# Kernel optimization log

Measured on AMD Instinct MI355X. Metric: run time of the kernel, lower is better.

The kernel has to match this reference:

```python
import jax, jax.numpy as jnp
import numpy as np

# Adaptive-LIF constants (Yin et al. spiking RNN, which this thesis repo builds on)
B_J0 = 0.01    # baseline threshold
BETA = 1.8     # adaptation strength
GAMMA = 0.5    # surrogate gradient scale
LENS = 0.5     # surrogate gaussian width
HIGHT = 0.15   # multi-gaussian side-lobe height
SCALE = 6.0    # side-lobe width multiplier


def _gaussian(x, mu, sigma):
    return jnp.exp(-((x - mu) ** 2) / (2.0 * sigma ** 2)) / (jnp.sqrt(2.0 * jnp.pi) * sigma)


@jax.custom_vjp
def spike_fn(v):
    # Heaviside spike with multi-gaussian surrogate gradient
    return (v > 0).astype(v.dtype)

def _spike_fwd(v):
    return spike_fn(v), v

def _spike_bwd(v, g):
    sg = (_gaussian(v, 0.0, LENS) * (1.0 + HIGHT)
          - _gaussian(v, LENS, SCALE * LENS) * HIGHT
          - _gaussian(v, -LENS, SCALE * LENS) * HIGHT)
    return (g * sg * GAMMA,)

spike_fn.defvjp(_spike_fwd, _spike_bwd)


def setup_inputs() -> dict:
    key = jax.random.key(0)
    ks = jax.random.split(key, 16)
    B, S, C, H, O = 256, 250, 700, 256, 20

    def lin(k, fan_in, shape):  # nn.Linear default init
        lim = 1.0 / np.sqrt(fan_in)
        return jax.random.uniform(k, shape, jnp.float32, -lim, lim)

    def tau(k, mean, std, shape):
        return jnp.clip(mean + std * jax.random.normal(k, shape, jnp.float32), 1.0, None)

    return {
        "x": jax.random.normal(ks[0], (B, S, C), jnp.float32),
        # forward spiking cell (tauM ~ N(20, ~5), tauAdp ~ N(200, ~50))
        "W_in_f": lin(ks[1], C, (C, H)), "b_in_f": lin(ks[2], C, (H,)),
        "W_rec_f": lin(ks[3], H, (H, H)), "b_rec_f": lin(ks[4], H, (H,)),
        "tau_m_f": tau(ks[5], 20.0, 5.0, (H,)),
        "tau_adp_f": tau(ks[6], 200.0, 50.0, (H,)),
        # backward spiking cell
        "W_in_b": lin(ks[7], C, (C, H)), "b_in_b": lin(ks[8], C, (H,)),
        "W_rec_b": lin(ks[9], H, (H, H)), "b_rec_b": lin(ks[10], H, (H,)),
        "tau_m_b": tau(ks[11], 20.0, 5.0, (H,)),
        "tau_adp_b": tau(ks[12], 200.0, 50.0, (H,)),
        # readout leaky integrator over concat(fw, bw) = 512 -> 20, tauM ~ N(3, 1)
        "W_out": lin(ks[13], 2 * H, (2 * H, O)), "b_out": lin(ks[14], 2 * H, (O,)),
        "tau_m_out": tau(ks[15], 3.0, 1.0, (O,)),
    }


def reference(x, W_in_f, b_in_f, W_rec_f, b_rec_f, tau_m_f, tau_adp_f,
              W_in_b, b_in_b, W_rec_b, b_rec_b, tau_m_b, tau_adp_b,
              W_out, b_out, tau_m_out):
    B, S, C = x.shape
    H = W_in_f.shape[1]
    O = W_out.shape[1]

    alpha_f = jnp.exp(-1.0 / tau_m_f); ro_f = jnp.exp(-1.0 / tau_adp_f)
    alpha_b = jnp.exp(-1.0 / tau_m_b); ro_b = jnp.exp(-1.0 / tau_adp_b)
    alpha_o = jnp.exp(-1.0 / tau_m_out)

    # Batch the feed-forward input projections over all timesteps: [S, B, H]
    proj_f = jnp.einsum("bsc,ch->sbh", x, W_in_f) + b_in_f
    proj_b = jnp.einsum("bsc,ch->sbh", x[:, ::-1], W_in_b) + b_in_b

    def cell(in_t, mem, spk, bb, W_rec, b_rec, alpha, ro):
        # mem_update_adp: adaptive threshold LIF
        d = in_t + spk @ W_rec + b_rec
        bb = ro * bb + (1.0 - ro) * spk
        thr = B_J0 + BETA * bb
        mem = mem * alpha + (1.0 - alpha) * d - thr * spk
        spk = spike_fn(mem - thr)
        return mem, spk, bb

    def step(carry, xs):
        mem_f, spk_f, bb_f, mem_b, spk_b, bb_b, mem_o = carry
        in_f, in_b = xs
        mem_f, spk_f, bb_f = cell(in_f, mem_f, spk_f, bb_f, W_rec_f, b_rec_f, alpha_f, ro_f)
        mem_b, spk_b, bb_b = cell(in_b, mem_b, spk_b, bb_b, W_rec_b, b_rec_b, alpha_b, ro_b)
        # readout integrator over concat(fw, bw) spikes (method=1 integrates every step)
        merged = jnp.concatenate([spk_f, spk_b], axis=-1)
        mem_o = mem_o * alpha_o + (1.0 - alpha_o) * (merged @ W_out + b_out)
        return (mem_f, spk_f, bb_f, mem_b, spk_b, bb_b, mem_o), None

    z = jnp.zeros((B, H), x.dtype)
    b0 = jnp.full((B, H), B_J0, x.dtype)
    carry0 = (z, z, b0, z, z, b0, jnp.zeros((B, O), x.dtype))
    carry, _ = jax.lax.scan(step, carry0, (proj_f, proj_b))
    return jax.nn.log_softmax(carry[-1], axis=-1)
```

## Files before the change

kernel.cpp:

```cpp
#include <hip/hip_runtime.h>
#include <cstdint>
#include <cstddef>

#define S_LEN 250
#define BATCH 256
#define CIN   700
#define HID   256
#define OUT_N 20
#define KSTEPS 22

typedef __attribute__((ext_vector_type(8))) short bf16x8;
typedef __attribute__((ext_vector_type(4))) float f32x4;

__device__ __forceinline__ ushort f2bf_rne(float f) {
    uint u = __float_as_uint(f);
    uint r = (u + 0x7FFFu + ((u >> 16) & 1u)) >> 16;
    return (ushort)r;
}
__device__ __forceinline__ float bf2f(ushort h) {
    return __uint_as_float(((uint)h) << 16);
}

__global__ __launch_bounds__(256) void proj_mfma(
    const float* __restrict__ x,
    const float* __restrict__ Wf, const float* __restrict__ Wb,
    const float* __restrict__ biasf, const float* __restrict__ biasb,
    float* __restrict__ P)
{
    __shared__ ushort AsH[128][40];
    __shared__ ushort AsL[128][40];
    __shared__ ushort BsH[128][40];
    __shared__ ushort BsL[128][40];

    const int nt = blockIdx.x;
    const int mt = blockIdx.y;
    const int m0 = mt * 128;
    const float* W   = (nt < 2) ? Wf : Wb;
    const float* bia = (nt < 2) ? biasf : biasb;
    const int wc0 = (nt & 1) * 128;

    const int tid  = threadIdx.x;
    const int lane = tid & 63;
    const int wv   = tid >> 6;
    const int wr   = wv >> 1;
    const int wc   = wv & 1;
    const int l15  = lane & 15;
    const int l4   = lane >> 4;

    const int as  = tid & 7;
    const int arr = tid >> 3;
    const int bcol = tid & 127;
    const int bkh  = tid >> 7;

    f32x4 acc[4][4];
#pragma unroll
    for (int i = 0; i < 4; i++)
#pragma unroll
        for (int j = 0; j < 4; j++)
            acc[i][j] = (f32x4){0.f, 0.f, 0.f, 0.f};

    for (int kt = 0; kt < KSTEPS; kt++) {
        const int k0 = kt * 32;

        float4 av[4];
        const int ka = k0 + as * 4;
        const bool aok = (ka + 3) < CIN;
#pragma unroll
        for (int i = 0; i < 4; i++) {
            av[i] = make_float4(0.f, 0.f, 0.f, 0.f);
            if (aok)
                av[i] = *(const float4*)&x[(size_t)(m0 + arr + 32 * i) * CIN + ka];
        }
        float bv[16];
#pragma unroll
        for (int j = 0; j < 16; j++) {
            const int kb = k0 + bkh * 16 + j;
            bv[j] = (kb < CIN) ? W[(size_t)kb * HID + wc0 + bcol] : 0.f;
        }

        __syncthreads();

#pragma unroll
        for (int i = 0; i < 4; i++) {
            const int row = arr + 32 * i;
            ushort4 h, l;
            h.x = f2bf_rne(av[i].x); l.x = f2bf_rne(__fsub_rn(av[i].x, bf2f(h.x)));
            h.y = f2bf_rne(av[i].y); l.y = f2bf_rne(__fsub_rn(av[i].y, bf2f(h.y)));
            h.z = f2bf_rne(av[i].z); l.z = f2bf_rne(__fsub_rn(av[i].z, bf2f(h.z)));
            h.w = f2bf_rne(av[i].w); l.w = f2bf_rne(__fsub_rn(av[i].w, bf2f(h.w)));
            *(ushort4*)&AsH[row][as * 4] = h;
            *(ushort4*)&AsL[row][as * 4] = l;
        }
#pragma unroll
        for (int q = 0; q < 4; q++) {
            ushort4 h, l;
            float v0 = bv[q * 4 + 0], v1 = bv[q * 4 + 1];
            float v2 = bv[q * 4 + 2], v3 = bv[q * 4 + 3];
            h.x = f2bf_rne(v0); l.x = f2bf_rne(__fsub_rn(v0, bf2f(h.x)));
            h.y = f2bf_rne(v1); l.y = f2bf_rne(__fsub_rn(v1, bf2f(h.y)));
            h.z = f2bf_rne(v2); l.z = f2bf_rne(__fsub_rn(v2, bf2f(h.z)));
            h.w = f2bf_rne(v3); l.w = f2bf_rne(__fsub_rn(v3, bf2f(h.w)));
            *(ushort4*)&BsH[bcol][bkh * 16 + q * 4] = h;
            *(ushort4*)&BsL[bcol][bkh * 16 + q * 4] = l;
        }
        __syncthreads();

        bf16x8 aH[4], aL[4], bH[4], bL[4];
#pragma unroll
        for (int f = 0; f < 4; f++) {
            aH[f] = *(const bf16x8*)&AsH[wr * 64 + f * 16 + l15][l4 * 8];
            aL[f] = *(const bf16x8*)&AsL[wr * 64 + f * 16 + l15][l4 * 8];
            bH[f] = *(const bf16x8*)&BsH[wc * 64 + f * 16 + l15][l4 * 8];
            bL[f] = *(const bf16x8*)&BsL[wc * 64 + f * 16 + l15][l4 * 8];
        }
#pragma unroll
        for (int fr = 0; fr < 4; fr++)
#pragma unroll
            for (int fc = 0; fc < 4; fc++) {
                acc[fr][fc] = __builtin_amdgcn_mfma_f32_16x16x32_bf16(
                    aH[fr], bH[fc], acc[fr][fc], 0, 0, 0);
                acc[fr][fc] = __builtin_amdgcn_mfma_f32_16x16x32_bf16(
                    aH[fr], bL[fc], acc[fr][fc], 0, 0, 0);
                acc[fr][fc] = __builtin_amdgcn_mfma_f32_16x16x32_bf16(
                    aL[fr], bH[fc], acc[fr][fc], 0, 0, 0);
            }
    }

#pragma unroll
    for (int fc = 0; fc < 4; fc++) {
        const float bvs = bia[wc0 + wc * 64 + fc * 16 + l15];
#pragma unroll
        for (int fr = 0; fr < 4; fr++) {
#pragma unroll
            for (int j = 0; j < 4; j++) {
                const int row = m0 + wr * 64 + fr * 16 + l4 * 4 + j;
                P[(size_t)row * 512 + nt * 128 + wc * 64 + fc * 16 + l15] =
                    __fadd_rn(acc[fr][fc][j], bvs);
            }
        }
    }
}

__global__ __launch_bounds__(512, 2) void scan_mfma(
    const float* __restrict__ P,
    const float* __restrict__ Wrecf, const float* __restrict__ brecf,
    const float* __restrict__ taumf, const float* __restrict__ tauaf,
    const float* __restrict__ Wrecb, const float* __restrict__ brecb,
    const float* __restrict__ taumb, const float* __restrict__ tauab,
    const float* __restrict__ Wout, const float* __restrict__ taumo,
    float* __restrict__ Pst)
{
    const int g  = blockIdx.x;
    const int d  = blockIdx.y;
    const int b0 = g * 16;
    const bool fw = (d == 0);

    const int tid  = threadIdx.x;
    const int lane = tid & 63;
    const int w    = tid >> 6;
    const int l15  = lane & 15;
    const int l4   = lane >> 4;

    __shared__ ushort Sp[2][16][264];

    {
        ushort* p = &Sp[0][0][0];
        for (int i = tid; i < 2 * 16 * 264; i += 512) p[i] = 0;
    }

    const float* Wrec = fw ? Wrecf : Wrecb;

    bf16x8 whf[8][2], wlf[8][2];
#pragma unroll
    for (int kt = 0; kt < 8; kt++)
#pragma unroll
        for (int ct = 0; ct < 2; ct++) {
            const int c = w * 32 + ct * 16 + l15;
#pragma unroll
            for (int j = 0; j < 8; j++) {
                const float v = Wrec[(size_t)(kt * 32 + l4 * 8 + j) * HID + c];
                const ushort h = f2bf_rne(v);
                const ushort l = f2bf_rne(__fsub_rn(v, bf2f(h)));
                whf[kt][ct][j] = (short)h;
                wlf[kt][ct][j] = (short)l;
            }
        }

    bf16x8 woh[2], wol[2];
#pragma unroll
    for (int t = 0; t < 2; t++) {
        const int o = t * 16 + l15;
#pragma unroll
        for (int j = 0; j < 8; j++) {
            float v = 0.f;
            if (o < OUT_N)
                v = Wout[(size_t)(d * HID + w * 32 + l4 * 8 + j) * OUT_N + o];
            const ushort h = f2bf_rne(v);
            const ushort l = f2bf_rne(__fsub_rn(v, bf2f(h)));
            woh[t][j] = (short)h;
            wol[t][j] = (short)l;
        }
    }

    float alpha_[2], ro_[2], omA_[2], omR_[2], brc_[2];
#pragma unroll
    for (int t = 0; t < 2; t++) {
        const int c = w * 32 + t * 16 + l15;
        alpha_[t] = expf(__fdiv_rn(-1.f, fw ? taumf[c] : taumb[c]));
        ro_[t]    = expf(__fdiv_rn(-1.f, fw ? tauaf[c] : tauab[c]));
        omA_[t]   = __fsub_rn(1.f, alpha_[t]);
        omR_[t]   = __fsub_rn(1.f, ro_[t]);
        brc_[t]   = fw ? brecf[c] : brecb[c];
    }
    float ao_[2], omo_[2];
#pragma unroll
    for (int t = 0; t < 2; t++) {
        const int o = t * 16 + l15;
        if (o < OUT_N) {
            ao_[t]  = expf(__fdiv_rn(-1.f, taumo[o]));
            omo_[t] = __fsub_rn(1.f, ao_[t]);
        } else { ao_[t] = 0.f; omo_[t] = 0.f; }
    }

    float mem[2][4], bbv[2][4], spkv[2][4], z[2][4];
#pragma unroll
    for (int t = 0; t < 2; t++)
#pragma unroll
        for (int j = 0; j < 4; j++) {
            mem[t][j] = 0.f; bbv[t][j] = 0.01f; spkv[t][j] = 0.f; z[t][j] = 0.f;
        }

    float pv[2][4];
    {
        const int srow = fw ? 0 : (S_LEN - 1);
#pragma unroll
        for (int t = 0; t < 2; t++)
#pragma unroll
            for (int j = 0; j < 4; j++)
                pv[t][j] = P[((size_t)(b0 + l4 * 4 + j) * S_LEN + srow) * 512
                             + d * HID + w * 32 + t * 16 + l15];
    }

    for (int s = 0; s < S_LEN; s++) {
        const int cur = s & 1, prev = cur ^ 1;

        float pvn[2][4];
        {
            const int sn  = s + 1;
            const int srn = fw ? (sn < S_LEN ? sn : S_LEN - 1)
                               : (sn < S_LEN ? (S_LEN - 1 - sn) : 0);
#pragma unroll
            for (int t = 0; t < 2; t++)
#pragma unroll
                for (int j = 0; j < 4; j++)
                    pvn[t][j] = P[((size_t)(b0 + l4 * 4 + j) * S_LEN + srn) * 512
                                  + d * HID + w * 32 + t * 16 + l15];
        }

        __syncthreads();

        f32x4 acc[2];
        acc[0] = (f32x4){0.f, 0.f, 0.f, 0.f};
        acc[1] = (f32x4){0.f, 0.f, 0.f, 0.f};
#pragma unroll
        for (int kt = 0; kt < 8; kt++) {
            const bf16x8 a = *(const bf16x8*)&Sp[prev][l15][kt * 32 + l4 * 8];
            acc[0] = __builtin_amdgcn_mfma_f32_16x16x32_bf16(a, whf[kt][0], acc[0], 0, 0, 0);
            acc[0] = __builtin_amdgcn_mfma_f32_16x16x32_bf16(a, wlf[kt][0], acc[0], 0, 0, 0);
            acc[1] = __builtin_amdgcn_mfma_f32_16x16x32_bf16(a, whf[kt][1], acc[1], 0, 0, 0);
            acc[1] = __builtin_amdgcn_mfma_f32_16x16x32_bf16(a, wlf[kt][1], acc[1], 0, 0, 0);
        }

#pragma unroll
        for (int t = 0; t < 2; t++) {
#pragma unroll
            for (int j = 0; j < 4; j++) {
                const float dd = __fadd_rn(__fadd_rn(pv[t][j], acc[t][j]), brc_[t]);
                bbv[t][j] = __fadd_rn(__fmul_rn(ro_[t], bbv[t][j]),
                                      __fmul_rn(omR_[t], spkv[t][j]));
                const float thr = __fadd_rn(0.01f, __fmul_rn(1.8f, bbv[t][j]));
                mem[t][j] = __fsub_rn(
                    __fadd_rn(__fmul_rn(mem[t][j], alpha_[t]),
                              __fmul_rn(omA_[t], dd)),
                    __fmul_rn(thr, spkv[t][j]));
                const bool sp = __fsub_rn(mem[t][j], thr) > 0.f;
                spkv[t][j] = sp ? 1.f : 0.f;
                Sp[cur][l4 * 4 + j][w * 32 + t * 16 + l15] =
                    sp ? (ushort)0x3F80 : (ushort)0;
            }
        }

        asm volatile("s_waitcnt lgkmcnt(0)" ::: "memory");
        __builtin_amdgcn_sched_barrier(0);

        {
            const bf16x8 ar = *(const bf16x8*)&Sp[cur][l15][w * 32 + l4 * 8];
            f32x4 S0 = (f32x4){0.f, 0.f, 0.f, 0.f};
            f32x4 S1 = (f32x4){0.f, 0.f, 0.f, 0.f};
            S0 = __builtin_amdgcn_mfma_f32_16x16x32_bf16(ar, woh[0], S0, 0, 0, 0);
            S0 = __builtin_amdgcn_mfma_f32_16x16x32_bf16(ar, wol[0], S0, 0, 0, 0);
            S1 = __builtin_amdgcn_mfma_f32_16x16x32_bf16(ar, woh[1], S1, 0, 0, 0);
            S1 = __builtin_amdgcn_mfma_f32_16x16x32_bf16(ar, wol[1], S1, 0, 0, 0);
#pragma unroll
            for (int j = 0; j < 4; j++) {
                z[0][j] = __fmaf_rn(ao_[0], z[0][j], __fmul_rn(omo_[0], S0[j]));
                z[1][j] = __fmaf_rn(ao_[1], z[1][j], __fmul_rn(omo_[1], S1[j]));
            }
        }

#pragma unroll
        for (int t = 0; t < 2; t++)
#pragma unroll
            for (int j = 0; j < 4; j++) pv[t][j] = pvn[t][j];
    }

    __syncthreads();

    float* stash = Pst + ((size_t)b0 * S_LEN) * 512 + d * HID;
#pragma unroll
    for (int j = 0; j < 4; j++) {
        const int r = l4 * 4 + j;
        const int idx0 = w * 320 + r * 16 + l15;
        stash[(size_t)(idx0 >> 8) * 512 + (idx0 & 255)] = z[0][j];
        if (l15 < 4) {
            const int idx1 = w * 320 + 256 + r * 4 + l15;
            stash[(size_t)(idx1 >> 8) * 512 + (idx1 & 255)] = z[1][j];
        }
    }
}

__global__ __launch_bounds__(64) void merge_out(
    const float* __restrict__ Pst, const float* __restrict__ bout,
    const float* __restrict__ taumo, float* __restrict__ out)
{
    const int bb = blockIdx.x;
    const int o  = threadIdx.x;
    const int g  = bb >> 4, r = bb & 15;

    float val = 0.f, v = -3.0e38f;
    if (o < OUT_N) {
        float tot = 0.f;
#pragma unroll
        for (int d2 = 0; d2 < 2; d2++) {
            const float* stash = Pst + ((size_t)(g * 16) * S_LEN) * 512 + d2 * HID;
#pragma unroll
            for (int w2 = 0; w2 < 8; w2++) {
                const int idx = (o < 16) ? (w2 * 320 + r * 16 + o)
                                         : (w2 * 320 + 256 + r * 4 + (o - 16));
                tot = __fadd_rn(tot, stash[(size_t)(idx >> 8) * 512 + (idx & 255)]);
            }
        }
        const float aS = expf(__fdiv_rn(-(float)S_LEN, taumo[o]));
        val = __fadd_rn(tot, __fmul_rn(bout[o], __fsub_rn(1.f, aS)));
        v = val;
    }
    float mx = v;
#pragma unroll
    for (int d2 = 1; d2 < 64; d2 <<= 1)
        mx = fmaxf(mx, __shfl_xor(mx, d2, 64));
    float e = (o < OUT_N) ? expf(__fsub_rn(val, mx)) : 0.f;
#pragma unroll
    for (int d2 = 1; d2 < 64; d2 <<= 1)
        e += __shfl_xor(e, d2, 64);
    if (o < OUT_N)
        out[(size_t)bb * OUT_N + o] =
            __fsub_rn(__fsub_rn(val, mx), logf(e));
}

extern "C" void kernel_launch(void* const* d_in, const int* in_sizes, int n_in,
                              void* d_out, int out_size, void* d_ws, size_t ws_size,
                              hipStream_t stream) {
    const float* x         = (const float*)d_in[0];
    const float* W_in_f    = (const float*)d_in[1];
    const float* b_in_f    = (const float*)d_in[2];
    const float* W_rec_f   = (const float*)d_in[3];
    const float* b_rec_f   = (const float*)d_in[4];
    const float* tau_m_f   = (const float*)d_in[5];
    const float* tau_adp_f = (const float*)d_in[6];
    const float* W_in_b    = (const float*)d_in[7];
    const float* b_in_b    = (const float*)d_in[8];
    const float* W_rec_b   = (const float*)d_in[9];
    const float* b_rec_b   = (const float*)d_in[10];
    const float* tau_m_b   = (const float*)d_in[11];
    const float* tau_adp_b = (const float*)d_in[12];
    const float* W_out     = (const float*)d_in[13];
    const float* b_out     = (const float*)d_in[14];
    const float* tau_m_o   = (const float*)d_in[15];
    float* out = (float*)d_out;
    float* P   = (float*)d_ws;

    proj_mfma<<<dim3(4, 500), dim3(256), 0, stream>>>(
        x, W_in_f, W_in_b, b_in_f, b_in_b, P);
    scan_mfma<<<dim3(16, 2), dim3(512), 0, stream>>>(
        P, W_rec_f, b_rec_f, tau_m_f, tau_adp_f,
        W_rec_b, b_rec_b, tau_m_b, tau_adp_b,
        W_out, tau_m_o, P);
    merge_out<<<dim3(BATCH), dim3(64), 0, stream>>>(
        P, b_out, tau_m_o, out);
}
```

Measured before the change: 517.7 us.

## Defer readout MFMA by one step, split accumulators, swizzle LDS, prefetch two steps

Moves the readout MFMA for step s-1 into step s's recurrent MFMA block, reading the previous spike buffer. This removes the separate lgkmcnt wait and sched barrier from the serial critical path, with one extra readout applied after the loop. It also splits the hi/lo accumulators to shorten MFMA dependency chains and swaps the padded LDS layout for an XOR swizzle to avoid bank conflicts. The P projection prefetch now runs two steps ahead to hide global load latency. The cost is more registers and some restructuring risk around the z update order, where the readout now lags by one step.

```diff
diff --git a/kernel.cpp b/kernel.cpp
--- a/kernel.cpp
+++ b/kernel.cpp
@@ -161,11 +161,11 @@
     const int l15  = lane & 15;
     const int l4   = lane >> 4;
 
-    __shared__ ushort Sp[2][16][264];
+    __shared__ ushort Sp[2][16][256];
 
     {
         ushort* p = &Sp[0][0][0];
-        for (int i = tid; i < 2 * 16 * 264; i += 512) p[i] = 0;
+        for (int i = tid; i < 2 * 16 * 256; i += 512) p[i] = 0;
     }
 
     const float* Wrec = fw ? Wrecf : Wrecb;
@@ -230,52 +230,96 @@
             mem[t][j] = 0.f; bbv[t][j] = 0.01f; spkv[t][j] = 0.f; z[t][j] = 0.f;
         }
 
-    float pv[2][4];
-    {
-        const int srow = fw ? 0 : (S_LEN - 1);
-#pragma unroll
-        for (int t = 0; t < 2; t++)
-#pragma unroll
-            for (int j = 0; j < 4; j++)
-                pv[t][j] = P[((size_t)(b0 + l4 * 4 + j) * S_LEN + srow) * 512
-                             + d * HID + w * 32 + t * 16 + l15];
-    }
+#define PROW(S_) (fw ? (((S_) < S_LEN) ? (S_) : (S_LEN - 1)) \
+                     : (((S_) < S_LEN) ? (S_LEN - 1 - (S_)) : 0))
+#define PLOAD(dst, S_) do {                                            \
+        const int srow_ = PROW(S_);                                    \
+        _Pragma("unroll")                                              \
+        for (int t_ = 0; t_ < 2; t_++)                                 \
+            _Pragma("unroll")                                          \
+            for (int j_ = 0; j_ < 4; j_++)                             \
+                dst[t_][j_] = P[((size_t)(b0 + l4 * 4 + j_) * S_LEN + srow_) * 512 \
+                                + d * HID + w * 32 + t_ * 16 + l15];   \
+    } while (0)
+
+    float pvC[2][4], pvN[2][4];
+    PLOAD(pvC, 0);
+    PLOAD(pvN, 1);
+
+    const int rsw = (l15 & 7) << 3;
 
     for (int s = 0; s < S_LEN; s++) {
         const int cur = s & 1, prev = cur ^ 1;
 
-        float pvn[2][4];
+        float pvL[2][4];
+        PLOAD(pvL, s + 2);
+
+        __syncthreads();
+
+        f32x4 accH[2], accL[2];
+        accH[0] = (f32x4){0.f, 0.f, 0.f, 0.f};
+        accH[1] = (f32x4){0.f, 0.f, 0.f, 0.f};
+        accL[0] = (f32x4){0.f, 0.f, 0.f, 0.f};
+        accL[1] = (f32x4){0.f, 0.f, 0.f, 0.f};
+
         {
-            const int sn  = s + 1;
-            const int srn = fw ? (sn < S_LEN ? sn : S_LEN - 1)
-                               : (sn < S_LEN ? (S_LEN - 1 - sn) : 0);
-#pragma unroll
-            for (int t = 0; t < 2; t++)
-#pragma unroll
-                for (int j = 0; j < 4; j++)
-                    pvn[t][j] = P[((size_t)(b0 + l4 * 4 + j) * S_LEN + srn) * 512
-                                  + d * HID + w * 32 + t * 16 + l15];
-        }
-
-        __syncthreads();
-
-        f32x4 acc[2];
-        acc[0] = (f32x4){0.f, 0.f, 0.f, 0.f};
-        acc[1] = (f32x4){0.f, 0.f, 0.f, 0.f};
-#pragma unroll
-        for (int kt = 0; kt < 8; kt++) {
-            const bf16x8 a = *(const bf16x8*)&Sp[prev][l15][kt * 32 + l4 * 8];
-            acc[0] = __builtin_amdgcn_mfma_f32_16x16x32_bf16(a, whf[kt][0], acc[0], 0, 0, 0);
-            acc[0] = __builtin_amdgcn_mfma_f32_16x16x32_bf16(a, wlf[kt][0], acc[0], 0, 0, 0);
-            acc[1] = __builtin_amdgcn_mfma_f32_16x16x32_bf16(a, whf[kt][1], acc[1], 0, 0, 0);
-            acc[1] = __builtin_amdgcn_mfma_f32_16x16x32_bf16(a, wlf[kt][1], acc[1], 0, 0, 0);
+            bf16x8 a0 = *(const bf16x8*)&Sp[prev][l15][(0 * 32 + l4 * 8) ^ rsw];
+            bf16x8 a1 = *(const bf16x8*)&Sp[prev][l15][(1 * 32 + l4 * 8) ^ rsw];
+            bf16x8 a2 = *(const bf16x8*)&Sp[prev][l15][(2 * 32 + l4 * 8) ^ rsw];
+            bf16x8 a3 = *(const bf16x8*)&Sp[prev][l15][(3 * 32 + l4 * 8) ^ rsw];
+            accH[0] = __builtin_amdgcn_mfma_f32_16x16x32_bf16(a0, whf[0][0], accH[0], 0, 0, 0);
+            accL[0] = __builtin_amdgcn_mfma_f32_16x16x32_bf16(a0, wlf[0][0], accL[0], 0, 0, 0);
+            accH[1] = __builtin_amdgcn_mfma_f32_16x16x32_bf16(a0, whf[0][1], accH[1], 0, 0, 0);
+            accL[1] = __builtin_amdgcn_mfma_f32_16x16x32_bf16(a0, wlf[0][1], accL[1], 0, 0, 0);
+            accH[0] = __builtin_amdgcn_mfma_f32_16x16x32_bf16(a1, whf[1][0], accH[0], 0, 0, 0);
+            accL[0] = __builtin_amdgcn_mfma_f32_16x16x32_bf16(a1, wlf[1][0], accL[0], 0, 0, 0);
+            accH[1] = __builtin_amdgcn_mfma_f32_16x16x32_bf16(a1, whf[1][1], accH[1], 0, 0, 0);
+            accL[1] = __builtin_amdgcn_mfma_f32_16x16x32_bf16(a1, wlf[1][1], accL[1], 0, 0, 0);
+            accH[0] = __builtin_amdgcn_mfma_f32_16x16x32_bf16(a2, whf[2][0], accH[0], 0, 0, 0);
+            accL[0] = __builtin_amdgcn_mfma_f32_16x16x32_bf16(a2, wlf[2][0], accL[0], 0, 0, 0);
+            accH[1] = __builtin_amdgcn_mfma_f32_16x16x32_bf16(a2, whf[2][1], accH[1], 0, 0, 0);
+            accL[1] = __builtin_amdgcn_mfma_f32_16x16x32_bf16(a2, wlf[2][1], accL[1], 0, 0, 0);
+            accH[0] = __builtin_amdgcn_mfma_f32_16x16x32_bf16(a3, whf[3][0], accH[0], 0, 0, 0);
+            accL[0] = __builtin_amdgcn_mfma_f32_16x16x32_bf16(a3, wlf[3][0], accL[0], 0, 0, 0);
+            accH[1] = __builtin_amdgcn_mfma_f32_16x16x32_bf16(a3, whf[3][1], accH[1], 0, 0, 0);
+            accL[1] = __builtin_amdgcn_mfma_f32_16x16x32_bf16(a3, wlf[3][1], accL[1], 0, 0, 0);
+        }
+        f32x4 S0 = (f32x4){0.f, 0.f, 0.f, 0.f};
+        f32x4 S1 = (f32x4){0.f, 0.f, 0.f, 0.f};
+        {
+            bf16x8 a4 = *(const bf16x8*)&Sp[prev][l15][(4 * 32 + l4 * 8) ^ rsw];
+            bf16x8 a5 = *(const bf16x8*)&Sp[prev][l15][(5 * 32 + l4 * 8) ^ rsw];
+            bf16x8 a6 = *(const bf16x8*)&Sp[prev][l15][(6 * 32 + l4 * 8) ^ rsw];
+            bf16x8 a7 = *(const bf16x8*)&Sp[prev][l15][(7 * 32 + l4 * 8) ^ rsw];
+            bf16x8 ar = *(const bf16x8*)&Sp[prev][l15][(w * 32 + l4 * 8) ^ rsw];
+            accH[0] = __builtin_amdgcn_mfma_f32_16x16x32_bf16(a4, whf[4][0], accH[0], 0, 0, 0);
+            accL[0] = __builtin_amdgcn_mfma_f32_16x16x32_bf16(a4, wlf[4][0], accL[0], 0, 0, 0);
+            accH[1] = __builtin_amdgcn_mfma_f32_16x16x32_bf16(a4, whf[4][1], accH[1], 0, 0, 0);
+            accL[1] = __builtin_amdgcn_mfma_f32_16x16x32_bf16(a4, wlf[4][1], accL[1], 0, 0, 0);
+            accH[0] = __builtin_amdgcn_mfma_f32_16x16x32_bf16(a5, whf[5][0], accH[0], 0, 0, 0);
+            accL[0] = __builtin_amdgcn_mfma_f32_16x16x32_bf16(a5, wlf[5][0], accL[0], 0, 0, 0);
+            accH[1] = __builtin_amdgcn_mfma_f32_16x16x32_bf16(a5, whf[5][1], accH[1], 0, 0, 0);
+            accL[1] = __builtin_amdgcn_mfma_f32_16x16x32_bf16(a5, wlf[5][1], accL[1], 0, 0, 0);
+            accH[0] = __builtin_amdgcn_mfma_f32_16x16x32_bf16(a6, whf[6][0], accH[0], 0, 0, 0);
+            accL[0] = __builtin_amdgcn_mfma_f32_16x16x32_bf16(a6, wlf[6][0], accL[0], 0, 0, 0);
+            accH[1] = __builtin_amdgcn_mfma_f32_16x16x32_bf16(a6, whf[6][1], accH[1], 0, 0, 0);
+            accL[1] = __builtin_amdgcn_mfma_f32_16x16x32_bf16(a6, wlf[6][1], accL[1], 0, 0, 0);
+            accH[0] = __builtin_amdgcn_mfma_f32_16x16x32_bf16(a7, whf[7][0], accH[0], 0, 0, 0);
+            accL[0] = __builtin_amdgcn_mfma_f32_16x16x32_bf16(a7, wlf[7][0], accL[0], 0, 0, 0);
+            accH[1] = __builtin_amdgcn_mfma_f32_16x16x32_bf16(a7, whf[7][1], accH[1], 0, 0, 0);
+            accL[1] = __builtin_amdgcn_mfma_f32_16x16x32_bf16(a7, wlf[7][1], accL[1], 0, 0, 0);
+            S0 = __builtin_amdgcn_mfma_f32_16x16x32_bf16(ar, woh[0], S0, 0, 0, 0);
+            S0 = __builtin_amdgcn_mfma_f32_16x16x32_bf16(ar, wol[0], S0, 0, 0, 0);
+            S1 = __builtin_amdgcn_mfma_f32_16x16x32_bf16(ar, woh[1], S1, 0, 0, 0);
+            S1 = __builtin_amdgcn_mfma_f32_16x16x32_bf16(ar, wol[1], S1, 0, 0, 0);
         }
 
 #pragma unroll
         for (int t = 0; t < 2; t++) {
 #pragma unroll
             for (int j = 0; j < 4; j++) {
-                const float dd = __fadd_rn(__fadd_rn(pv[t][j], acc[t][j]), brc_[t]);
+                const float accv = __fadd_rn(accH[t][j], accL[t][j]);
+                const float dd = __fadd_rn(__fadd_rn(pvC[t][j], accv), brc_[t]);
                 bbv[t][j] = __fadd_rn(__fmul_rn(ro_[t], bbv[t][j]),
                                       __fmul_rn(omR_[t], spkv[t][j]));
                 const float thr = __fadd_rn(0.01f, __fmul_rn(1.8f, bbv[t][j]));
@@ -285,36 +329,44 @@
                     __fmul_rn(thr, spkv[t][j]));
                 const bool sp = __fsub_rn(mem[t][j], thr) > 0.f;
                 spkv[t][j] = sp ? 1.f : 0.f;
-                Sp[cur][l4 * 4 + j][w * 32 + t * 16 + l15] =
+                const int row = l4 * 4 + j;
+                Sp[cur][row][(w * 32 + t * 16 + l15) ^ ((row & 7) << 3)] =
                     sp ? (ushort)0x3F80 : (ushort)0;
             }
         }
 
-        asm volatile("s_waitcnt lgkmcnt(0)" ::: "memory");
-        __builtin_amdgcn_sched_barrier(0);
-
-        {
-            const bf16x8 ar = *(const bf16x8*)&Sp[cur][l15][w * 32 + l4 * 8];
-            f32x4 S0 = (f32x4){0.f, 0.f, 0.f, 0.f};
-            f32x4 S1 = (f32x4){0.f, 0.f, 0.f, 0.f};
-            S0 = __builtin_amdgcn_mfma_f32_16x16x32_bf16(ar, woh[0], S0, 0, 0, 0);
-            S0 = __builtin_amdgcn_mfma_f32_16x16x32_bf16(ar, wol[0], S0, 0, 0, 0);
-            S1 = __builtin_amdgcn_mfma_f32_16x16x32_bf16(ar, woh[1], S1, 0, 0, 0);
-            S1 = __builtin_amdgcn_mfma_f32_16x16x32_bf16(ar, wol[1], S1, 0, 0, 0);
+#pragma unroll
+        for (int j = 0; j < 4; j++) {
+            z[0][j] = __fmaf_rn(ao_[0], z[0][j], __fmul_rn(omo_[0], S0[j]));
+            z[1][j] = __fmaf_rn(ao_[1], z[1][j], __fmul_rn(omo_[1], S1[j]));
+        }
+
+#pragma unroll
+        for (int t = 0; t < 2; t++)
 #pragma unroll
             for (int j = 0; j < 4; j++) {
-                z[0][j] = __fmaf_rn(ao_[0], z[0][j], __fmul_rn(omo_[0], S0[j]));
-                z[1][j] = __fmaf_rn(ao_[1], z[1][j], __fmul_rn(omo_[1], S1[j]));
-            }
-        }
-
-#pragma unroll
-        for (int t = 0; t < 2; t++)
-#pragma unroll
-            for (int j = 0; j < 4; j++) pv[t][j] = pvn[t][j];
+                pvC[t][j] = pvN[t][j];
+                pvN[t][j] = pvL[t][j];
+            }
     }
 
     __syncthreads();
+
+    {
+        const int lastbuf = (S_LEN - 1) & 1;
+        bf16x8 ar = *(const bf16x8*)&Sp[lastbuf][l15][(w * 32 + l4 * 8) ^ rsw];
+        f32x4 S0 = (f32x4){0.f, 0.f, 0.f, 0.f};
+        f32x4 S1 = (f32x4){0.f, 0.f, 0.f, 0.f};
+        S0 = __builtin_amdgcn_mfma_f32_16x16x32_bf16(ar, woh[0], S0, 0, 0, 0);
+        S0 = __builtin_amdgcn_mfma_f32_16x16x32_bf16(ar, wol[0], S0, 0, 0, 0);
+        S1 = __builtin_amdgcn_mfma_f32_16x16x32_bf16(ar, woh[1], S1, 0, 0, 0);
+        S1 = __builtin_amdgcn_mfma_f32_16x16x32_bf16(ar, wol[1], S1, 0, 0, 0);
+#pragma unroll
+        for (int j = 0; j < 4; j++) {
+            z[0][j] = __fmaf_rn(ao_[0], z[0][j], __fmul_rn(omo_[0], S0[j]));
+            z[1][j] = __fmaf_rn(ao_[1], z[1][j], __fmul_rn(omo_[1], S1[j]));
+        }
+    }
 
     float* stash = Pst + ((size_t)b0 * S_LEN) * 512 + d * HID;
 #pragma unroll
@@ -327,6 +379,8 @@
             stash[(size_t)(idx1 >> 8) * 512 + (idx1 & 255)] = z[1][j];
         }
     }
+#undef PLOAD
+#undef PROW
 }
 
 __global__ __launch_bounds__(64) void merge_out(
```

Result: slower. 875.6 us (+69.1%).

## Widen projection tile to 256 columns, pre-split weights, and software-pipeline loads

Applied to the files above, without the earlier changes.

The projection GEMM now computes a 128x256 tile per block, so x is read and split into bf16 hi/lo twice instead of four times. A new prep kernel converts the input weights once into transposed bf16 hi/lo planes in workspace, which removes the per-block weight conversion and the strided global reads. The K loop prefetches the next tile into registers while the MFMAs run on the current one. The cost is more accumulator registers (128 floats per thread) and more LDS, which may lower occupancy, plus one extra kernel launch.

```diff
diff --git a/kernel.cpp b/kernel.cpp
--- a/kernel.cpp
+++ b/kernel.cpp
@@ -8,8 +8,10 @@
 #define HID   256
 #define OUT_N 20
 #define KSTEPS 22
+#define KPAD  704
 
 typedef __attribute__((ext_vector_type(8))) short bf16x8;
+typedef __attribute__((ext_vector_type(8))) unsigned short u16x8;
 typedef __attribute__((ext_vector_type(4))) float f32x4;
 
 __device__ __forceinline__ ushort f2bf_rne(float f) {
@@ -21,23 +23,40 @@
     return __uint_as_float(((uint)h) << 16);
 }
 
+__global__ __launch_bounds__(512) void w_prep(
+    const float* __restrict__ Wf, const float* __restrict__ Wb,
+    ushort* __restrict__ Wth, ushort* __restrict__ Wtl)
+{
+    const int k = blockIdx.x;
+    const int c = threadIdx.x;
+    float v = 0.f;
+    if (k < CIN)
+        v = (c < HID) ? Wf[(size_t)k * HID + c]
+                      : Wb[(size_t)k * HID + (c - HID)];
+    const ushort h = f2bf_rne(v);
+    const ushort l = f2bf_rne(__fsub_rn(v, bf2f(h)));
+    Wth[(size_t)c * KPAD + k] = h;
+    Wtl[(size_t)c * KPAD + k] = l;
+}
+
+template<bool PREW>
 __global__ __launch_bounds__(256) void proj_mfma(
     const float* __restrict__ x,
     const float* __restrict__ Wf, const float* __restrict__ Wb,
     const float* __restrict__ biasf, const float* __restrict__ biasb,
+    const ushort* __restrict__ Wth, const ushort* __restrict__ Wtl,
     float* __restrict__ P)
 {
     __shared__ ushort AsH[128][40];
     __shared__ ushort AsL[128][40];
-    __shared__ ushort BsH[128][40];
-    __shared__ ushort BsL[128][40];
+    __shared__ ushort BsH[256][40];
+    __shared__ ushort BsL[256][40];
 
     const int nt = blockIdx.x;
     const int mt = blockIdx.y;
     const int m0 = mt * 128;
-    const float* W   = (nt < 2) ? Wf : Wb;
-    const float* bia = (nt < 2) ? biasf : biasb;
-    const int wc0 = (nt & 1) * 128;
+    const float* W   = nt ? Wb : Wf;
+    const float* bia = nt ? biasb : biasf;
 
     const int tid  = threadIdx.x;
     const int lane = tid & 63;
@@ -49,21 +68,20 @@
 
     const int as  = tid & 7;
     const int arr = tid >> 3;
-    const int bcol = tid & 127;
-    const int bkh  = tid >> 7;
-
-    f32x4 acc[4][4];
+
+    f32x4 acc[4][8];
 #pragma unroll
     for (int i = 0; i < 4; i++)
 #pragma unroll
-        for (int j = 0; j < 4; j++)
+        for (int j = 0; j < 8; j++)
             acc[i][j] = (f32x4){0.f, 0.f, 0.f, 0.f};
 
-    for (int kt = 0; kt < KSTEPS; kt++) {
-        const int k0 = kt * 32;
-
-        float4 av[4];
-        const int ka = k0 + as * 4;
+    float4 av[4];
+    float bv[32];
+    u16x8 bh[4], bl[4];
+
+    auto LOADT = [&](int K0) {
+        const int ka = K0 + as * 4;
         const bool aok = (ka + 3) < CIN;
 #pragma unroll
         for (int i = 0; i < 4; i++) {
@@ -71,15 +89,23 @@
             if (aok)
                 av[i] = *(const float4*)&x[(size_t)(m0 + arr + 32 * i) * CIN + ka];
         }
-        float bv[16];
-#pragma unroll
-        for (int j = 0; j < 16; j++) {
-            const int kb = k0 + bkh * 16 + j;
-            bv[j] = (kb < CIN) ? W[(size_t)kb * HID + wc0 + bcol] : 0.f;
-        }
-
-        __syncthreads();
-
+        if constexpr (PREW) {
+            const size_t base = (size_t)(nt * HID + tid) * KPAD + K0;
+#pragma unroll
+            for (int q = 0; q < 4; q++) {
+                bh[q] = *(const u16x8*)&Wth[base + q * 8];
+                bl[q] = *(const u16x8*)&Wtl[base + q * 8];
+            }
+        } else {
+#pragma unroll
+            for (int j = 0; j < 32; j++) {
+                const int kb = K0 + j;
+                bv[j] = (kb < CIN) ? W[(size_t)kb * HID + tid] : 0.f;
+            }
+        }
+    };
+
+    auto WRITET = [&]() {
 #pragma unroll
         for (int i = 0; i < 4; i++) {
             const int row = arr + 32 * i;
@@ -91,50 +117,68 @@
             *(ushort4*)&AsH[row][as * 4] = h;
             *(ushort4*)&AsL[row][as * 4] = l;
         }
-#pragma unroll
-        for (int q = 0; q < 4; q++) {
-            ushort4 h, l;
-            float v0 = bv[q * 4 + 0], v1 = bv[q * 4 + 1];
-            float v2 = bv[q * 4 + 2], v3 = bv[q * 4 + 3];
-            h.x = f2bf_rne(v0); l.x = f2bf_rne(__fsub_rn(v0, bf2f(h.x)));
-            h.y = f2bf_rne(v1); l.y = f2bf_rne(__fsub_rn(v1, bf2f(h.y)));
-            h.z = f2bf_rne(v2); l.z = f2bf_rne(__fsub_rn(v2, bf2f(h.z)));
-            h.w = f2bf_rne(v3); l.w = f2bf_rne(__fsub_rn(v3, bf2f(h.w)));
-            *(ushort4*)&BsH[bcol][bkh * 16 + q * 4] = h;
-            *(ushort4*)&BsL[bcol][bkh * 16 + q * 4] = l;
-        }
+        if constexpr (PREW) {
+#pragma unroll
+            for (int q = 0; q < 4; q++) {
+                *(u16x8*)&BsH[tid][q * 8] = bh[q];
+                *(u16x8*)&BsL[tid][q * 8] = bl[q];
+            }
+        } else {
+#pragma unroll
+            for (int q = 0; q < 8; q++) {
+                ushort4 h, l;
+                float v0 = bv[q * 4 + 0], v1 = bv[q * 4 + 1];
+                float v2 = bv[q * 4 + 2], v3 = bv[q * 4 + 3];
+                h.x = f2bf_rne(v0); l.x = f2bf_rne(__fsub_rn(v0, bf2f(h.x)));
+                h.y = f2bf_rne(v1); l.y = f2bf_rne(__fsub_rn(v1, bf2f(h.y)));
+                h.z = f2bf_rne(v2); l.z = f2bf_rne(__fsub_rn(v2, bf2f(h.z)));
+                h.w = f2bf_rne(v3); l.w = f2bf_rne(__fsub_rn(v3, bf2f(h.w)));
+                *(ushort4*)&BsH[tid][q * 4] = h;
+                *(ushort4*)&BsL[tid][q * 4] = l;
+            }
+        }
+    };
+
+    LOADT(0);
+    WRITET();
+
+    for (int kt = 0; kt < KSTEPS; kt++) {
         __syncthreads();
-
-        bf16x8 aH[4], aL[4], bH[4], bL[4];
-#pragma unroll
-        for (int f = 0; f < 4; f++) {
-            aH[f] = *(const bf16x8*)&AsH[wr * 64 + f * 16 + l15][l4 * 8];
-            aL[f] = *(const bf16x8*)&AsL[wr * 64 + f * 16 + l15][l4 * 8];
-            bH[f] = *(const bf16x8*)&BsH[wc * 64 + f * 16 + l15][l4 * 8];
-            bL[f] = *(const bf16x8*)&BsL[wc * 64 + f * 16 + l15][l4 * 8];
-        }
-#pragma unroll
-        for (int fr = 0; fr < 4; fr++)
-#pragma unroll
-            for (int fc = 0; fc < 4; fc++) {
+        if (kt + 1 < KSTEPS)
+            LOADT((kt + 1) * 32);
+
+#pragma unroll
+        for (int fc = 0; fc < 8; fc++) {
+            const bf16x8 bHf = *(const bf16x8*)&BsH[wc * 128 + fc * 16 + l15][l4 * 8];
+            const bf16x8 bLf = *(const bf16x8*)&BsL[wc * 128 + fc * 16 + l15][l4 * 8];
+#pragma unroll
+            for (int fr = 0; fr < 4; fr++) {
+                const bf16x8 aHf = *(const bf16x8*)&AsH[wr * 64 + fr * 16 + l15][l4 * 8];
+                const bf16x8 aLf = *(const bf16x8*)&AsL[wr * 64 + fr * 16 + l15][l4 * 8];
                 acc[fr][fc] = __builtin_amdgcn_mfma_f32_16x16x32_bf16(
-                    aH[fr], bH[fc], acc[fr][fc], 0, 0, 0);
+                    aHf, bHf, acc[fr][fc], 0, 0, 0);
                 acc[fr][fc] = __builtin_amdgcn_mfma_f32_16x16x32_bf16(
-                    aH[fr], bL[fc], acc[fr][fc], 0, 0, 0);
+                    aHf, bLf, acc[fr][fc], 0, 0, 0);
                 acc[fr][fc] = __builtin_amdgcn_mfma_f32_16x16x32_bf16(
-                    aL[fr], bH[fc], acc[fr][fc], 0, 0, 0);
-            }
-    }
-
-#pragma unroll
-    for (int fc = 0; fc < 4; fc++) {
-        const float bvs = bia[wc0 + wc * 64 + fc * 16 + l15];
+                    aLf, bHf, acc[fr][fc], 0, 0, 0);
+            }
+        }
+
+        __syncthreads();
+        if (kt + 1 < KSTEPS)
+            WRITET();
+    }
+
+#pragma unroll
+    for (int fc = 0; fc < 8; fc++) {
+        const int col = wc * 128 + fc * 16 + l15;
+        const float bvs = bia[col];
 #pragma unroll
         for (int fr = 0; fr < 4; fr++) {
 #pragma unroll
             for (int j = 0; j < 4; j++) {
                 const int row = m0 + wr * 64 + fr * 16 + l4 * 4 + j;
-                P[(size_t)row * 512 + nt * 128 + wc * 64 + fc * 16 + l15] =
+                P[(size_t)row * 512 + nt * HID + col] =
                     __fadd_rn(acc[fr][fc][j], bvs);
             }
         }
@@ -244,17 +288,16 @@
     for (int s = 0; s < S_LEN; s++) {
         const int cur = s & 1, prev = cur ^ 1;
 
-        float pvn[2][4];
+        float pv_next[2][4];
         {
-            const int sn  = s + 1;
-            const int srn = fw ? (sn < S_LEN ? sn : S_LEN - 1)
-                               : (sn < S_LEN ? (S_LEN - 1 - sn) : 0);
+            const int sn   = (s + 1 < S_LEN) ? s + 1 : S_LEN - 1;
+            const int srow = fw ? sn : (S_LEN - 1 - sn);
 #pragma unroll
             for (int t = 0; t < 2; t++)
 #pragma unroll
                 for (int j = 0; j < 4; j++)
-                    pvn[t][j] = P[((size_t)(b0 + l4 * 4 + j) * S_LEN + srn) * 512
-                                  + d * HID + w * 32 + t * 16 + l15];
+                    pv_next[t][j] = P[((size_t)(b0 + l4 * 4 + j) * S_LEN + srow) * 512
+                                      + d * HID + w * 32 + t * 16 + l15];
         }
 
         __syncthreads();
@@ -311,7 +354,7 @@
 #pragma unroll
         for (int t = 0; t < 2; t++)
 #pragma unroll
-            for (int j = 0; j < 4; j++) pv[t][j] = pvn[t][j];
+            for (int j = 0; j < 4; j++) pv[t][j] = pv_next[t][j];
     }
 
     __syncthreads();
@@ -389,8 +432,20 @@
     float* out = (float*)d_out;
     float* P   = (float*)d_ws;
 
-    proj_mfma<<<dim3(4, 500), dim3(256), 0, stream>>>(
-        x, W_in_f, W_in_b, b_in_f, b_in_b, P);
+    const size_t needP = (size_t)BATCH * S_LEN * 512 * sizeof(float);
+    const size_t planeW = (size_t)512 * KPAD;
+    ushort* Wth = (ushort*)((char*)d_ws + needP);
+    ushort* Wtl = Wth + planeW;
+    const bool prew = (ws_size >= needP + 2 * planeW * sizeof(ushort));
+
+    if (prew) {
+        w_prep<<<dim3(KPAD), dim3(512), 0, stream>>>(W_in_f, W_in_b, Wth, Wtl);
+        proj_mfma<true><<<dim3(2, 500), dim3(256), 0, stream>>>(
+            x, W_in_f, W_in_b, b_in_f, b_in_b, Wth, Wtl, P);
+    } else {
+        proj_mfma<false><<<dim3(2, 500), dim3(256), 0, stream>>>(
+            x, W_in_f, W_in_b, b_in_f, b_in_b, nullptr, nullptr, P);
+    }
     scan_mfma<<<dim3(16, 2), dim3(512), 0, stream>>>(
         P, W_rec_f, b_rec_f, tau_m_f, tau_adp_f,
         W_rec_b, b_rec_b, tau_m_b, tau_adp_b,
```

After: 502.3 us. 3.0% less time.
